# Kernel tuning notes

Measured on AMD Instinct MI355X. Metric: run time of the kernel, lower is better.

The kernel has to match this reference:

```python
import jax, jax.numpy as jnp
import numpy as np

N, C = 1048576, 128
ALPHA, GAMA = 0.25, 2


def setup_inputs() -> dict:
    key = jax.random.key(0)
    k1, k2 = jax.random.split(key)
    preds = jax.random.normal(k1, (N, C), dtype=jnp.float32)
    label_idx = jax.random.randint(k2, (N,), 0, C)
    labels = jax.nn.one_hot(label_idx, C, dtype=jnp.int32)  # one-hot, matches labels[i][j]==1 test
    return {"preds": preds, "labels": labels}


def reference(preds, labels):
    # t2[i] = -preds[i, label_i]  (gather via one-hot)
    lbl_logit = jnp.sum(preds * labels.astype(preds.dtype), axis=1)  # [N]
    t2 = -lbl_logit
    # t1[i] = sum_j exp(preds[i, j])  (original uses unstabilized sum-exp)
    t1 = jnp.sum(jnp.exp(preds), axis=1)  # [N]
    # per-row focal loss: alpha * (1 - p)^gama * CE, with p = exp(label_logit)/sumexp
    p = jnp.exp(-t2) / t1
    per_row = ALPHA * jnp.power(1.0 - p, GAMA) * (t2 + jnp.log(t1))
    # the final python loop is an incremental running mean => plain mean
    return jnp.mean(per_row)
```

## Files before the change

kernel.cpp:

```cpp
#include <hip/hip_runtime.h>

#define FL_N 1048576
#define FL_C 128
#define FL_ALPHA 0.25f

constexpr int BLOCKS = 2048;
constexpr int TPB    = 256;
constexpr int WAVES_PER_BLOCK = TPB / 64;
constexpr int ROWS_PER_WAVE   = 8;
constexpr int ROWBLOCKS       = FL_N / ROWS_PER_WAVE;

using f32x4 = __attribute__((ext_vector_type(4))) float;
using i32x4 = __attribute__((ext_vector_type(4))) int;

__device__ __forceinline__ float exp4_sum(f32x4 p) {
    return __expf(p.x) + __expf(p.y) + __expf(p.z) + __expf(p.w);
}
__device__ __forceinline__ float dot4(f32x4 p, i32x4 l) {
    return p.x * (float)l.x + p.y * (float)l.y + p.z * (float)l.z + p.w * (float)l.w;
}

template<int CTRL>
__device__ __forceinline__ float dpp_xadd(float x) {
    int m = __builtin_amdgcn_update_dpp(0, __float_as_int(x), CTRL, 0xF, 0xF, true);
    return x + __int_as_float(m);
}
__device__ __forceinline__ float group8_sum(float x) {
    x = dpp_xadd<0xB1>(x);
    x = dpp_xadd<0x4E>(x);
    x = dpp_xadd<0x141>(x);
    return x;
}

__global__ __launch_bounds__(TPB) void focal_partial(
    const float* __restrict__ preds,
    const int*   __restrict__ labels,
    float*       __restrict__ partial)
{
    const int tid  = threadIdx.x;
    const int wave = tid >> 6;
    const int lane = tid & 63;

    const int wavesTotal = gridDim.x * WAVES_PER_BLOCK;
    const int gwave      = blockIdx.x * WAVES_PER_BLOCK + wave;

    const int laneOff = (lane >> 3) * FL_C + (lane & 7) * 4;

    float acc = 0.0f;

    for (int rb = gwave; rb < ROWBLOCKS; rb += wavesTotal) {
        size_t base = (size_t)rb * (ROWS_PER_WAVE * FL_C) + laneOff;
        const f32x4* pp = reinterpret_cast<const f32x4*>(preds + base);
        const i32x4* lp = reinterpret_cast<const i32x4*>(labels + base);

        f32x4 p0 = __builtin_nontemporal_load(pp + 0);
        f32x4 p1 = __builtin_nontemporal_load(pp + 8);
        f32x4 p2 = __builtin_nontemporal_load(pp + 16);
        f32x4 p3 = __builtin_nontemporal_load(pp + 24);
        i32x4 l0 = __builtin_nontemporal_load(lp + 0);
        i32x4 l1 = __builtin_nontemporal_load(lp + 8);
        i32x4 l2 = __builtin_nontemporal_load(lp + 16);
        i32x4 l3 = __builtin_nontemporal_load(lp + 24);

        float se = exp4_sum(p0) + exp4_sum(p1) + exp4_sum(p2) + exp4_sum(p3);
        float ll = dot4(p0, l0) + dot4(p1, l1) + dot4(p2, l2) + dot4(p3, l3);

        se = group8_sum(se);
        ll = group8_sum(ll);

        float t1 = se;
        float pr = __expf(ll) / t1;
        float om = 1.0f - pr;
        acc += FL_ALPHA * om * om * (__logf(t1) - ll);
    }

    #pragma unroll
    for (int m = 32; m >= 1; m >>= 1)
        acc += __shfl_xor(acc, m, 64);

    __shared__ float smem[WAVES_PER_BLOCK];
    if (lane == 0) smem[wave] = acc;
    __syncthreads();
    if (tid == 0) {
        float s = 0.0f;
        #pragma unroll
        for (int w = 0; w < WAVES_PER_BLOCK; ++w) s += smem[w];
        partial[blockIdx.x] = s;
    }
}

__global__ __launch_bounds__(256) void focal_final(
    const float* __restrict__ partial,
    float*       __restrict__ out)
{
    const int tid  = threadIdx.x;
    const int wave = tid >> 6;
    const int lane = tid & 63;

    float acc = 0.0f;
    for (int i = tid; i < BLOCKS; i += 256) acc += partial[i];

    #pragma unroll
    for (int m = 32; m >= 1; m >>= 1)
        acc += __shfl_xor(acc, m, 64);

    __shared__ float smem[4];
    if (lane == 0) smem[wave] = acc;
    __syncthreads();
    if (tid == 0) {
        float s = smem[0] + smem[1] + smem[2] + smem[3];
        out[0] = s * (1.0f / (8.0f * (float)FL_N));
    }
}

extern "C" void kernel_launch(void* const* d_in, const int* in_sizes, int n_in,
                              void* d_out, int out_size, void* d_ws, size_t ws_size,
                              hipStream_t stream)
{
    const float* preds  = (const float*)d_in[0];
    const int*   labels = (const int*)d_in[1];
    float*       out    = (float*)d_out;
    float*       part   = (float*)d_ws;

    focal_partial<<<BLOCKS, TPB, 0, stream>>>(preds, labels, part);
    focal_final<<<1, 256, 0, stream>>>(part, out);
}
```

Before: 919.9 us.

## Assign each row to 32 contiguous lanes and drop nontemporal loads

Each load instruction now covers two whole rows across the wave, so every wave-wide load touches 1 KB of contiguous memory instead of eight strided 128-byte segments. The row reduction grows from an 8-lane DPP sum to a 32-lane sum, adding a row_shr DPP step and a cross-16 shuffle. Each lane computes four focal terms per iteration. Both 32-lane halves hold every row's term, so the final scale changes to divide by 32N. Nontemporal hints are replaced with plain loads. This adds reduction work per row in exchange for better coalescing.

```diff
diff --git a/kernel.cpp b/kernel.cpp
--- a/kernel.cpp
+++ b/kernel.cpp
@@ -7,8 +7,8 @@
 constexpr int BLOCKS = 2048;
 constexpr int TPB    = 256;
 constexpr int WAVES_PER_BLOCK = TPB / 64;
-constexpr int ROWS_PER_WAVE   = 8;
-constexpr int ROWBLOCKS       = FL_N / ROWS_PER_WAVE;
+constexpr int ROWS_PER_ITER   = 8;
+constexpr int ROWBLOCKS       = FL_N / ROWS_PER_ITER;
 
 using f32x4 = __attribute__((ext_vector_type(4))) float;
 using i32x4 = __attribute__((ext_vector_type(4))) int;
@@ -25,11 +25,19 @@
     int m = __builtin_amdgcn_update_dpp(0, __float_as_int(x), CTRL, 0xF, 0xF, true);
     return x + __int_as_float(m);
 }
-__device__ __forceinline__ float group8_sum(float x) {
+__device__ __forceinline__ float group32_sum(float x) {
     x = dpp_xadd<0xB1>(x);
     x = dpp_xadd<0x4E>(x);
     x = dpp_xadd<0x141>(x);
+    x = dpp_xadd<0x140>(x);
+    x += __shfl_xor(x, 16, 64);
     return x;
+}
+
+__device__ __forceinline__ float focal_term(float se, float ll) {
+    float pr = __expf(ll) / se;
+    float om = 1.0f - pr;
+    return FL_ALPHA * om * om * (__logf(se) - ll);
 }
 
 __global__ __launch_bounds__(TPB) void focal_partial(
@@ -44,34 +52,32 @@
     const int wavesTotal = gridDim.x * WAVES_PER_BLOCK;
     const int gwave      = blockIdx.x * WAVES_PER_BLOCK + wave;
 
-    const int laneOff = (lane >> 3) * FL_C + (lane & 7) * 4;
-
     float acc = 0.0f;
 
     for (int rb = gwave; rb < ROWBLOCKS; rb += wavesTotal) {
-        size_t base = (size_t)rb * (ROWS_PER_WAVE * FL_C) + laneOff;
-        const f32x4* pp = reinterpret_cast<const f32x4*>(preds + base);
+        size_t base = (size_t)rb * (ROWS_PER_ITER * FL_C) + (size_t)lane * 4;
+        const f32x4* pp = reinterpret_cast<const f32x4*>(preds  + base);
         const i32x4* lp = reinterpret_cast<const i32x4*>(labels + base);
 
-        f32x4 p0 = __builtin_nontemporal_load(pp + 0);
-        f32x4 p1 = __builtin_nontemporal_load(pp + 8);
-        f32x4 p2 = __builtin_nontemporal_load(pp + 16);
-        f32x4 p3 = __builtin_nontemporal_load(pp + 24);
-        i32x4 l0 = __builtin_nontemporal_load(lp + 0);
-        i32x4 l1 = __builtin_nontemporal_load(lp + 8);
-        i32x4 l2 = __builtin_nontemporal_load(lp + 16);
-        i32x4 l3 = __builtin_nontemporal_load(lp + 24);
+        f32x4 p0 = pp[0];
+        f32x4 p1 = pp[64];
+        f32x4 p2 = pp[128];
+        f32x4 p3 = pp[192];
+        i32x4 l0 = lp[0];
+        i32x4 l1 = lp[64];
+        i32x4 l2 = lp[128];
+        i32x4 l3 = lp[192];
 
-        float se = exp4_sum(p0) + exp4_sum(p1) + exp4_sum(p2) + exp4_sum(p3);
-        float ll = dot4(p0, l0) + dot4(p1, l1) + dot4(p2, l2) + dot4(p3, l3);
+        float e0 = exp4_sum(p0), e1 = exp4_sum(p1), e2 = exp4_sum(p2), e3 = exp4_sum(p3);
+        float d0 = dot4(p0, l0), d1 = dot4(p1, l1), d2 = dot4(p2, l2), d3 = dot4(p3, l3);
 
-        se = group8_sum(se);
-        ll = group8_sum(ll);
+        e0 = group32_sum(e0);  d0 = group32_sum(d0);
+        e1 = group32_sum(e1);  d1 = group32_sum(d1);
+        e2 = group32_sum(e2);  d2 = group32_sum(d2);
+        e3 = group32_sum(e3);  d3 = group32_sum(d3);
 
-        float t1 = se;
-        float pr = __expf(ll) / t1;
-        float om = 1.0f - pr;
-        acc += FL_ALPHA * om * om * (__logf(t1) - ll);
+        acc += focal_term(e0, d0) + focal_term(e1, d1)
+             + focal_term(e2, d2) + focal_term(e3, d3);
     }
 
     #pragma unroll
@@ -109,7 +115,7 @@
     __syncthreads();
     if (tid == 0) {
         float s = smem[0] + smem[1] + smem[2] + smem[3];
-        out[0] = s * (1.0f / (8.0f * (float)FL_N));
+        out[0] = s * (1.0f / (32.0f * (float)FL_N));
     }
 }
 
```

New measurement: 970.8 us. 1.06x slower.
